# Performance work log

Measured on AMD Instinct MI355X. Metric: run time of the kernel, lower is better.

Reference implementation:

```python
import jax, jax.numpy as jnp
import numpy as np

IN_F, OUT_F, BLOCK, NBLK = 1024, 4096, 256, 16
TOPK = NBLK // 4  # 4, as in forward: n_blocks // 4


def setup_inputs() -> dict:
    key = jax.random.key(0)
    ks = jax.random.split(key, 7)
    s = 1.0 / np.sqrt(IN_F)
    s2 = 1.0 / np.sqrt(OUT_F)
    return {
        "x": jax.random.normal(ks[0], (4, 4096, IN_F), jnp.float32),
        "router_w": jax.random.uniform(ks[1], (NBLK, IN_F), jnp.float32, -s, s),
        "router_b": jax.random.uniform(ks[2], (NBLK,), jnp.float32, -s, s),
        "w1": jax.random.uniform(ks[3], (OUT_F, IN_F), jnp.float32, -s, s),
        "b1": jax.random.uniform(ks[4], (OUT_F,), jnp.float32, -s, s),
        "w2": jax.random.uniform(ks[5], (IN_F, OUT_F), jnp.float32, -s2, s2),
        "b2": jax.random.uniform(ks[6], (IN_F,), jnp.float32, -s2, s2),
    }


def reference(x, router_w, router_b, w1, b1, w2, b2):
    x_shape = x.shape
    xf = x.reshape(-1, IN_F)  # [N, d]
    n = xf.shape[0]
    # router: Linear + softmax, then top-k block selection per token
    prob = jax.nn.softmax(xf @ router_w.T + router_b, axis=-1)  # [N, n_blocks]
    _, idx = jax.lax.top_k(prob, TOPK)  # [N, k]
    mask = jnp.zeros((n, NBLK), bool).at[jnp.arange(n)[:, None], idx].set(True)
    # RoutedLinearRow: per-block fc1, zeros at unselected blocks
    w1b = w1.reshape(NBLK, BLOCK, IN_F)
    b1b = b1.reshape(NBLK, BLOCK)
    h = jnp.einsum('nd,ibd->nib', xf, w1b) + b1b  # [N, n_blocks, block]
    h = jnp.where(mask[:, :, None], h, jnp.zeros((), h.dtype))
    h = jax.nn.relu(h)
    # RoutedLinearCol: only selected blocks contribute
    w2b = w2.reshape(IN_F, NBLK, BLOCK)
    y = jnp.einsum('nib,dib->nd', jnp.where(mask[:, :, None], h, 0.0), w2b) + b2
    return y.reshape(x_shape)
```

## Files before the change

### kernel.cpp

```cpp
#include <hip/hip_runtime.h>
#include <hip/hip_bf16.h>

#define NTOK   16384
#define INF    1024
#define OUTF   4096
#define NBLK   16
#define BLKSZ  256
#define KTOP   4

typedef short bf16x8 __attribute__((ext_vector_type(8)));
typedef float f32x4 __attribute__((ext_vector_type(4)));
typedef unsigned short u16x8 __attribute__((ext_vector_type(8)));

__device__ __forceinline__ unsigned short f2bf(float f) {
  unsigned u = __float_as_uint(f);
  u += 0x7FFFu + ((u >> 16) & 1u);
  return (unsigned short)(u >> 16);
}

__device__ __forceinline__ void load_lds16(const void* g, void* l) {
  __builtin_amdgcn_global_load_lds(
      (const __attribute__((address_space(1))) unsigned int*)g,
      (__attribute__((address_space(3))) unsigned int*)l, 16, 0, 0);
}

__device__ __forceinline__ double shfl_xor_d(double v, int m) {
  long long l = __double_as_longlong(v);
  int lo = (int)(l & 0xFFFFFFFFll), hi = (int)(l >> 32);
  lo = __shfl_xor(lo, m);
  hi = __shfl_xor(hi, m);
  return __longlong_as_double(((long long)hi << 32) | (unsigned long long)(unsigned)lo);
}

__device__ __forceinline__ int pi_perm(int j) {
  return (j & 128) | ((j & 7) << 4) | ((j >> 3) & 15);
}

__global__ void k_zero(unsigned* __restrict__ list32, unsigned* __restrict__ counts) {
  int i = blockIdx.x * 256 + threadIdx.x;
  if (i < 33792) list32[i] = 0;
  else if (i < 33808) counts[i - 33792] = 0;
}

__global__ __launch_bounds__(256) void k_convert(
    const float* __restrict__ w1, const float* __restrict__ w2,
    const float* __restrict__ b1, unsigned short* __restrict__ w1b,
    unsigned short* __restrict__ w2p, float* __restrict__ b1p) {
  const size_t stride = (size_t)gridDim.x * 256;
  for (size_t i = (size_t)blockIdx.x * 256 + threadIdx.x; i < 1573376; i += stride) {
    if (i < 1048576) {
      float4 v = ((const float4*)w1)[i];
      ushort4 o;
      o.x = f2bf(v.x); o.y = f2bf(v.y); o.z = f2bf(v.z); o.w = f2bf(v.w);
      ((ushort4*)w1b)[i] = o;
    } else if (i < 1572864) {
      const size_t g = i - 1048576;
      const int d = (int)(g >> 9);
      const int rest = (int)(g & 511);
      const int jg = rest * 8;
      const int blk = jg >> 8;
      const int j0 = jg & 255;
      const float* src = w2 + (size_t)d * 4096 + blk * 256;
      u16x8 o;
#pragma unroll
      for (int ni = 0; ni < 8; ++ni) o[ni] = f2bf(src[pi_perm(j0 + ni)]);
      *(u16x8*)(w2p + (size_t)d * 4096 + jg) = o;
    } else {
      const int idx = (int)(i - 1572864);
      const int jg = idx * 8;
      const int blk = jg >> 8;
      const int j0 = jg & 255;
      const float* src = b1 + blk * 256;
      float o[8];
#pragma unroll
      for (int ni = 0; ni < 8; ++ni) o[ni] = src[pi_perm(j0 + ni)];
      float4* dst = (float4*)(b1p + jg);
      dst[0] = make_float4(o[0], o[1], o[2], o[3]);
      dst[1] = make_float4(o[4], o[5], o[6], o[7]);
    }
  }
}

__global__ __launch_bounds__(256) void k_router(
    const float* __restrict__ x, const float* __restrict__ rw,
    const float* __restrict__ rb, unsigned* __restrict__ tok_blocks,
    unsigned* __restrict__ counts, unsigned short* __restrict__ xb) {
  __shared__ float4 rwl[4096];
  const int tid = threadIdx.x;
  const float4* rw4 = (const float4*)rw;
  for (int i = tid; i < 4096; i += 256) rwl[i] = rw4[i];
  __syncthreads();

  const int n = blockIdx.x * 32 + (tid >> 3);
  const int q = tid & 7;
  double p[16];
#pragma unroll
  for (int j = 0; j < 16; ++j) p[j] = 0.0;
  const float4* xr = (const float4*)(x + (size_t)n * INF);
  ushort4* xbr = (ushort4*)(xb + (size_t)n * INF);
#pragma unroll 4
  for (int i = 0; i < 32; ++i) {
    const int d4 = q + i * 8;
    const float4 xv = xr[d4];
    ushort4 o;
    o.x = f2bf(xv.x); o.y = f2bf(xv.y); o.z = f2bf(xv.z); o.w = f2bf(xv.w);
    xbr[d4] = o;
#pragma unroll
    for (int j = 0; j < 16; ++j) {
      const float4 wv = rwl[j * 256 + d4];
      p[j] = fma((double)xv.x, (double)wv.x, p[j]);
      p[j] = fma((double)xv.y, (double)wv.y, p[j]);
      p[j] = fma((double)xv.z, (double)wv.z, p[j]);
      p[j] = fma((double)xv.w, (double)wv.w, p[j]);
    }
  }
#pragma unroll
  for (int j = 0; j < 16; ++j) {
    double v = p[j];
    v += shfl_xor_d(v, 1);
    v += shfl_xor_d(v, 2);
    v += shfl_xor_d(v, 4);
    p[j] = v + (double)rb[j];
  }

  __syncthreads();
  unsigned* hist = (unsigned*)rwl;
  if (tid < 16) hist[tid] = 0;
  __syncthreads();

  if (q == 0) {
    unsigned packed = 0;
#pragma unroll
    for (int j = 0; j < 16; ++j) {
      int r = 0;
#pragma unroll
      for (int j2 = 0; j2 < 16; ++j2)
        r += (int)((p[j2] > p[j]) | ((p[j2] == p[j]) & (j2 < j)));
      if (r < KTOP) packed |= (unsigned)j << (8 * r);
    }
    tok_blocks[n] = packed;
    atomicAdd(&hist[packed & 15u], 1u);
    atomicAdd(&hist[(packed >> 8) & 15u], 1u);
    atomicAdd(&hist[(packed >> 16) & 15u], 1u);
    atomicAdd(&hist[(packed >> 24) & 15u], 1u);
  }
  __syncthreads();
  if (tid < 16 && hist[tid]) atomicAdd(&counts[tid], hist[tid]);
}

__global__ void k_scan(const unsigned* __restrict__ counts, unsigned* __restrict__ off,
                       unsigned* __restrict__ cursors) {
  if (threadIdx.x == 0 && blockIdx.x == 0) {
    unsigned o = 0;
    for (int i = 0; i < 16; ++i) {
      off[i] = o; cursors[i] = o;
      o += (counts[i] + 127u) & ~127u;
    }
    off[16] = o;
  }
}

__global__ __launch_bounds__(256) void k_build(
    const unsigned* __restrict__ tok_blocks, unsigned* __restrict__ cursors,
    unsigned short* __restrict__ list, unsigned* __restrict__ inv) {
  const int n = blockIdx.x * 256 + threadIdx.x;
  const unsigned packed = tok_blocks[n];
  const int lane = threadIdx.x & 63;
  for (int b = 0; b < 16; ++b) {
    int r = -1;
#pragma unroll
    for (int q = 0; q < 4; ++q)
      if (((packed >> (8 * q)) & 15u) == (unsigned)b) r = q;
    unsigned long long m = __ballot(r >= 0);
    if (m) {
      int leader = __ffsll((unsigned long long)m) - 1;
      unsigned base = 0;
      if (lane == leader) base = atomicAdd(&cursors[b], (unsigned)__popcll(m));
      base = (unsigned)__shfl((int)base, leader);
      if (r >= 0) {
        unsigned pos = base + (unsigned)__popcll(m & ((1ull << lane) - 1ull));
        list[pos] = (unsigned short)n;
        inv[(size_t)n * 4 + r] = pos;
      }
    }
  }
}

__global__ __launch_bounds__(512, 1) void k_ffn(
    const unsigned short* __restrict__ xb, const unsigned short* __restrict__ w1b,
    const unsigned short* __restrict__ w2p, const float* __restrict__ b1p,
    const unsigned short* __restrict__ list, const unsigned* __restrict__ counts,
    const unsigned* __restrict__ off, unsigned short* __restrict__ part) {
  __shared__ __align__(16) char lds[163840];
  char* const As0 = lds + 65536;
  char* const As1 = lds + 81920;
  char* const Bs0 = lds + 98304;
  char* const Bs1 = lds + 131072;

  const int bid0 = blockIdx.x;
  const int bid = (bid0 & 7) * 256 + (bid0 >> 3);
  const int blk = bid >> 7;
  const int tile = bid & 127;
  const unsigned cnt = counts[blk];
  if ((unsigned)(tile * 128) >= cnt) return;
  const unsigned goff = off[blk] + tile * 128;

  const int tid = threadIdx.x;
  const int lane = tid & 63;
  const int wid = tid >> 6;
  const int wr = wid >> 1;
  const int wc = wid & 1;
  const int asl = tid & 7;
  const int c16 = lane & 15;

  const unsigned tok0 = list[goff + (tid >> 3)];
  const unsigned tok1 = list[goff + 64 + (tid >> 3)];
  const int arow0 = tid >> 3;
  const int arow1 = 64 + arow0;

#define STAGE_A(buf, k0)                                                        \
  {                                                                             \
    load_lds16(xb + (size_t)tok0 * INF + (k0) + (asl ^ (arow0 & 7)) * 8,        \
               (buf) + (wid * 64) * 16);                                        \
    load_lds16(xb + (size_t)tok1 * INF + (k0) + (asl ^ (arow1 & 7)) * 8,        \
               (buf) + (512 + wid * 64) * 16);                                  \
  }

#define STAGE_B1(buf, k0)                                                       \
  _Pragma("unroll")                                                             \
  for (int r = 0; r < 4; ++r) {                                                 \
    const int row = (r * 512 + tid) >> 3;                                       \
    load_lds16(w1b + ((size_t)(blk * 256 + row)) * INF + (k0) +                 \
                   (asl ^ (row & 7)) * 8,                                       \
               (buf) + (r * 512 + wid * 64) * 16);                              \
  }

#define COMPUTE_A(abuf, bbuf)                                                   \
  _Pragma("unroll")                                                             \
  for (int ks = 0; ks < 2; ++ks) {                                              \
    const int kc = ks * 4 + (lane >> 4);                                        \
    bf16x8 a[2], b[8];                                                          \
    _Pragma("unroll")                                                           \
    for (int mi = 0; mi < 2; ++mi) {                                            \
      const int row = wr * 32 + mi * 16 + (lane & 15);                          \
      a[mi] = *(const bf16x8*)((abuf) + row * 128 + ((kc ^ (row & 7)) << 4));   \
    }                                                                           \
    _Pragma("unroll")                                                           \
    for (int ni = 0; ni < 8; ++ni) {                                            \
      const int row = wc * 128 + ni * 16 + (lane & 15);                         \
      b[ni] = *(const bf16x8*)((bbuf) + row * 128 + ((kc ^ (row & 7)) << 4));   \
    }                                                                           \
    _Pragma("unroll")                                                           \
    for (int mi = 0; mi < 2; ++mi)                                              \
      _Pragma("unroll")                                                         \
      for (int ni = 0; ni < 8; ++ni)                                            \
        acc[mi][ni] =                                                           \
            __builtin_amdgcn_mfma_f32_16x16x32_bf16(a[mi], b[ni], acc[mi][ni], 0, 0, 0); \
  }

  f32x4 acc[2][8] = {};
  STAGE_A(As0, 0);
  STAGE_B1(Bs0, 0);
  __syncthreads();
#pragma unroll 1
  for (int kk = 0; kk < 8; ++kk) {
    const int k0 = kk * 128;
    STAGE_A(As1, k0 + 64);
    STAGE_B1(Bs1, k0 + 64);
    COMPUTE_A(As0, Bs0);
    __syncthreads();
    if (kk < 7) {
      STAGE_A(As0, k0 + 128);
      STAGE_B1(Bs0, k0 + 128);
    }
    COMPUTE_A(As1, Bs1);
    __syncthreads();
  }

#define STAGE_B2(buf, it)                                                       \
  {                                                                             \
    const int ns2 = (it) >> 2, k02 = ((it) & 3) * 64;                           \
    _Pragma("unroll")                                                           \
    for (int r = 0; r < 4; ++r) {                                               \
      const int row = (r * 512 + tid) >> 3;                                     \
      load_lds16(w2p + (size_t)(ns2 * 256 + row) * OUTF + blk * 256 + k02 +     \
                     (asl ^ (row & 7)) * 8,                                     \
                 (buf) + (r * 512 + wid * 64) * 16);                            \
    }                                                                           \
  }

#define COMPUTE_B(bbuf, k02)                                                    \
  _Pragma("unroll")                                                             \
  for (int ks = 0; ks < 2; ++ks) {                                              \
    const int kc = ks * 4 + (lane >> 4);                                        \
    bf16x8 a[2], b[8];                                                          \
    _Pragma("unroll")                                                           \
    for (int mi = 0; mi < 2; ++mi) {                                            \
      const int row = wr * 32 + mi * 16 + (lane & 15);                          \
      a[mi] = *(const bf16x8*)(lds + row * 512 + (k02) * 2 +                    \
                               ((kc ^ (row & 7)) << 4));                        \
    }                                                                           \
    _Pragma("unroll")                                                           \
    for (int ni = 0; ni < 8; ++ni) {                                            \
      const int row = wc * 128 + ni * 16 + (lane & 15);                         \
      b[ni] = *(const bf16x8*)((bbuf) + row * 128 + ((kc ^ (row & 7)) << 4));   \
    }                                                                           \
    _Pragma("unroll")                                                           \
    for (int mi = 0; mi < 2; ++mi)                                              \
      _Pragma("unroll")                                                         \
      for (int ni = 0; ni < 8; ++ni)                                            \
        acc2[mi][ni] =                                                          \
            __builtin_amdgcn_mfma_f32_16x16x32_bf16(a[mi], b[ni], acc2[mi][ni], 0, 0, 0); \
  }

  STAGE_B2(Bs0, 0);

  {
    const float4* bp = (const float4*)(b1p + blk * 256 + wc * 128 + c16 * 8);
    const float4 bv0 = bp[0], bv1 = bp[1];
    const float bvv[8] = {bv0.x, bv0.y, bv0.z, bv0.w, bv1.x, bv1.y, bv1.z, bv1.w};
    const int chunk = wc * 16 + c16;
    const int cslot = (chunk & ~7);
    const int clow  = (chunk & 7);
#pragma unroll
    for (int mi = 0; mi < 2; ++mi) {
#pragma unroll
      for (int i = 0; i < 4; ++i) {
        const int row = wr * 32 + mi * 16 + (lane >> 4) * 4 + i;
        u16x8 wv;
#pragma unroll
        for (int ni = 0; ni < 8; ++ni) {
          float v = acc[mi][ni][i] + bvv[ni];
          v = v > 0.f ? v : 0.f;
          wv[ni] = f2bf(v);
        }
        *(u16x8*)(lds + row * 512 + ((cslot | (clow ^ (row & 7))) << 4)) = wv;
      }
    }
  }
  __syncthreads();

#pragma unroll 1
  for (int ns = 0; ns < 4; ++ns) {
    f32x4 acc2[2][8] = {};
    const int it0 = ns * 4;
    STAGE_B2(Bs1, it0 + 1);
    COMPUTE_B(Bs0, 0);
    __syncthreads();
    STAGE_B2(Bs0, it0 + 2);
    COMPUTE_B(Bs1, 64);
    __syncthreads();
    STAGE_B2(Bs1, it0 + 3);
    COMPUTE_B(Bs0, 128);
    __syncthreads();
    if (ns < 3) STAGE_B2(Bs0, it0 + 4);
    COMPUTE_B(Bs1, 192);
    __syncthreads();
#pragma unroll
    for (int mi = 0; mi < 2; ++mi) {
#pragma unroll
      for (int i = 0; i < 4; ++i) {
        const int row = wr * 32 + mi * 16 + (lane >> 4) * 4 + i;
        u16x8 wv;
#pragma unroll
        for (int ni = 0; ni < 8; ++ni) wv[ni] = f2bf(acc2[mi][ni][i]);
        *(u16x8*)(part + (size_t)(goff + row) * 1024 + ns * 256 + wc * 128 + c16 * 8) = wv;
      }
    }
  }
#undef STAGE_A
#undef STAGE_B1
#undef STAGE_B2
#undef COMPUTE_A
#undef COMPUTE_B
}

__global__ __launch_bounds__(256) void k_reduce(const unsigned short* __restrict__ part,
                                                const unsigned* __restrict__ inv,
                                                const float* __restrict__ b2,
                                                float* __restrict__ out) {
  __shared__ float lds[8 * 1028];
  const int tid = threadIdx.x;
  const int tok0 = blockIdx.x * 8;
  const int tok_l = tid >> 5;
  const int l32 = tid & 31;

  const uint4 iv = *(const uint4*)(inv + (size_t)(tok0 + tok_l) * 4);
  const unsigned prow[4] = {iv.x, iv.y, iv.z, iv.w};

#pragma unroll
  for (int g = 0; g < 4; ++g) {
    const int idx = g * 32 + l32;
    const int p0 = idx * 8;
    float s[8] = {0.f, 0.f, 0.f, 0.f, 0.f, 0.f, 0.f, 0.f};
#pragma unroll
    for (int sl = 0; sl < 4; ++sl) {
      u16x8 v = *(const u16x8*)(part + (size_t)prow[sl] * 1024 + p0);
#pragma unroll
      for (int j = 0; j < 8; ++j)
        s[j] += __uint_as_float((unsigned)(unsigned short)v[j] << 16);
    }
    const int ns = idx >> 5, wcb = (idx >> 4) & 1, cc = idx & 15;
#pragma unroll
    for (int ni = 0; ni < 8; ++ni)
      lds[tok_l * 1028 + ns * 256 + wcb * 128 + ni * 16 + cc] = s[ni];
  }
  __syncthreads();
  const float4 b2v = ((const float4*)b2)[tid];
#pragma unroll
  for (int r = 0; r < 8; ++r) {
    f32x4 lv = *(f32x4*)&lds[r * 1028 + tid * 4];
    float4 o = make_float4(lv[0] + b2v.x, lv[1] + b2v.y, lv[2] + b2v.z, lv[3] + b2v.w);
    *(float4*)(out + (size_t)(tok0 + r) * 1024 + tid * 4) = o;
  }
}

extern "C" void kernel_launch(void* const* d_in, const int* in_sizes, int n_in,
                              void* d_out, int out_size, void* d_ws, size_t ws_size,
                              hipStream_t stream) {
  const float* x  = (const float*)d_in[0];
  const float* rw = (const float*)d_in[1];
  const float* rb = (const float*)d_in[2];
  const float* w1 = (const float*)d_in[3];
  const float* b1 = (const float*)d_in[4];
  const float* w2 = (const float*)d_in[5];
  const float* b2 = (const float*)d_in[6];
  float* out = (float*)d_out;

  char* ws = (char*)d_ws;
  unsigned short* part = (unsigned short*)(ws);
  unsigned short* xb   = (unsigned short*)(ws + 138412032);
  unsigned short* w1b  = (unsigned short*)(ws + 171966464);
  unsigned short* w2p  = (unsigned short*)(ws + 180355072);
  unsigned* tokb       = (unsigned*)(ws + 188743680);
  unsigned short* list = (unsigned short*)(ws + 188809216);
  unsigned* inv        = (unsigned*)(ws + 188944384);
  float* b1p           = (float*)(ws + 189206528);
  unsigned* counts     = (unsigned*)(ws + 189222912);
  unsigned* off        = (unsigned*)(ws + 189222976);
  unsigned* cursors    = (unsigned*)(ws + 189223104);

  k_zero<<<dim3(133), dim3(256), 0, stream>>>((unsigned*)list, counts);
  k_convert<<<dim3(1024), dim3(256), 0, stream>>>(w1, w2, b1, w1b, w2p, b1p);
  k_router<<<dim3(512), dim3(256), 0, stream>>>(x, rw, rb, tokb, counts, xb);
  k_scan<<<dim3(1), dim3(64), 0, stream>>>(counts, off, cursors);
  k_build<<<dim3(64), dim3(256), 0, stream>>>(tokb, cursors, list, inv);
  k_ffn<<<dim3(2048), dim3(512), 0, stream>>>(xb, w1b, w2p, b1p, list, counts, off, part);
  k_reduce<<<dim3(2048), dim3(256), 0, stream>>>(part, inv, b2, out);
}
```

Before: 266.7 us.

## Triple-buffer FFN tiles with K=32 steps and one barrier per step

Rewrites both GEMM phases of the routed FFN kernel to use a three-deep LDS ring of K=32 slices in place of double-buffered K=64 slices. Explicit vmcnt waits and a single s_barrier per step replace the paired __syncthreads, so global-to-LDS loads for step t+2 are in flight while step t computes. The swizzle changes to a 64-byte row layout and total LDS drops. This shortens each MFMA burst per barrier and relies on hand-tuned vmcnt counts being correct, which is fragile.

```diff
diff --git a/kernel.cpp b/kernel.cpp
--- a/kernel.cpp
+++ b/kernel.cpp
@@ -191,11 +191,7 @@
     const unsigned short* __restrict__ w2p, const float* __restrict__ b1p,
     const unsigned short* __restrict__ list, const unsigned* __restrict__ counts,
     const unsigned* __restrict__ off, unsigned short* __restrict__ part) {
-  __shared__ __align__(16) char lds[163840];
-  char* const As0 = lds + 65536;
-  char* const As1 = lds + 81920;
-  char* const Bs0 = lds + 98304;
-  char* const Bs1 = lds + 131072;
+  __shared__ __align__(16) char lds[139264];
 
   const int bid0 = blockIdx.x;
   const int bid = (bid0 & 7) * 256 + (bid0 >> 3);
@@ -210,110 +206,106 @@
   const int wid = tid >> 6;
   const int wr = wid >> 1;
   const int wc = wid & 1;
-  const int asl = tid & 7;
   const int c16 = lane & 15;
-
-  const unsigned tok0 = list[goff + (tid >> 3)];
-  const unsigned tok1 = list[goff + 64 + (tid >> 3)];
-  const int arow0 = tid >> 3;
-  const int arow1 = 64 + arow0;
-
-#define STAGE_A(buf, k0)                                                        \
+  const int kc4 = lane >> 4;
+
+  const unsigned tokA = list[goff + (tid >> 2)];
+  const int aChunk = (tid & 3) ^ ((tid >> 3) & 3);
+
+#define VMF asm volatile("" ::: "memory")
+#define BAR __builtin_amdgcn_s_barrier()
+
+#define STAGE_A(buf, k0_)                                                       \
   {                                                                             \
-    load_lds16(xb + (size_t)tok0 * INF + (k0) + (asl ^ (arow0 & 7)) * 8,        \
-               (buf) + (wid * 64) * 16);                                        \
-    load_lds16(xb + (size_t)tok1 * INF + (k0) + (asl ^ (arow1 & 7)) * 8,        \
-               (buf) + (512 + wid * 64) * 16);                                  \
-  }
-
-#define STAGE_B1(buf, k0)                                                       \
-  _Pragma("unroll")                                                             \
-  for (int r = 0; r < 4; ++r) {                                                 \
-    const int row = (r * 512 + tid) >> 3;                                       \
-    load_lds16(w1b + ((size_t)(blk * 256 + row)) * INF + (k0) +                 \
-                   (asl ^ (row & 7)) * 8,                                       \
-               (buf) + (r * 512 + wid * 64) * 16);                              \
-  }
-
-#define COMPUTE_A(abuf, bbuf)                                                   \
-  _Pragma("unroll")                                                             \
-  for (int ks = 0; ks < 2; ++ks) {                                              \
-    const int kc = ks * 4 + (lane >> 4);                                        \
+    load_lds16(xb + (size_t)tokA * 1024 + (k0_) + aChunk * 8, (buf) + tid * 16);\
+    _Pragma("unroll")                                                           \
+    for (int l = 0; l < 2; ++l) {                                               \
+      const int idx = l * 512 + tid;                                            \
+      load_lds16(w1b + (size_t)(blk * 256 + (idx >> 2)) * 1024 + (k0_) +        \
+                     (((idx & 3) ^ ((idx >> 3) & 3)) * 8),                      \
+                 (buf) + 8192 + idx * 16);                                      \
+    }                                                                           \
+  }
+
+#define COMPUTE_A(buf)                                                          \
+  {                                                                             \
     bf16x8 a[2], b[8];                                                          \
     _Pragma("unroll")                                                           \
     for (int mi = 0; mi < 2; ++mi) {                                            \
       const int row = wr * 32 + mi * 16 + (lane & 15);                          \
-      a[mi] = *(const bf16x8*)((abuf) + row * 128 + ((kc ^ (row & 7)) << 4));   \
+      a[mi] = *(const bf16x8*)((buf) + row * 64 +                               \
+                               ((kc4 ^ ((row >> 1) & 3)) << 4));                \
     }                                                                           \
     _Pragma("unroll")                                                           \
     for (int ni = 0; ni < 8; ++ni) {                                            \
       const int row = wc * 128 + ni * 16 + (lane & 15);                         \
-      b[ni] = *(const bf16x8*)((bbuf) + row * 128 + ((kc ^ (row & 7)) << 4));   \
+      b[ni] = *(const bf16x8*)((buf) + 8192 + row * 64 +                        \
+                               ((kc4 ^ ((row >> 1) & 3)) << 4));                \
     }                                                                           \
     _Pragma("unroll")                                                           \
     for (int mi = 0; mi < 2; ++mi)                                              \
       _Pragma("unroll")                                                         \
       for (int ni = 0; ni < 8; ++ni)                                            \
-        acc[mi][ni] =                                                           \
-            __builtin_amdgcn_mfma_f32_16x16x32_bf16(a[mi], b[ni], acc[mi][ni], 0, 0, 0); \
-  }
-
+        acc[mi][ni] = __builtin_amdgcn_mfma_f32_16x16x32_bf16(a[mi], b[ni],     \
+                                                   acc[mi][ni], 0, 0, 0);       \
+  }
+
+  char* bA0 = lds + 65536;
+  char* bA1 = lds + 90112;
+  char* bA2 = lds + 114688;
   f32x4 acc[2][8] = {};
-  STAGE_A(As0, 0);
-  STAGE_B1(Bs0, 0);
-  __syncthreads();
+  STAGE_A(bA0, 0);
+  STAGE_A(bA1, 32);
 #pragma unroll 1
-  for (int kk = 0; kk < 8; ++kk) {
-    const int k0 = kk * 128;
-    STAGE_A(As1, k0 + 64);
-    STAGE_B1(Bs1, k0 + 64);
-    COMPUTE_A(As0, Bs0);
-    __syncthreads();
-    if (kk < 7) {
-      STAGE_A(As0, k0 + 128);
-      STAGE_B1(Bs0, k0 + 128);
-    }
-    COMPUTE_A(As1, Bs1);
-    __syncthreads();
-  }
-
-#define STAGE_B2(buf, it)                                                       \
+  for (int t = 0; t < 32; ++t) {
+    if (t < 31) { asm volatile("s_waitcnt vmcnt(3)" ::: "memory"); }
+    else        { asm volatile("s_waitcnt vmcnt(0)" ::: "memory"); }
+    BAR; VMF;
+    if (t < 30) STAGE_A(bA2, (t + 2) * 32);
+    COMPUTE_A(bA0);
+    char* tmp = bA0; bA0 = bA1; bA1 = bA2; bA2 = tmp;
+  }
+
+#define STAGE_B(buf, it_)                                                       \
   {                                                                             \
-    const int ns2 = (it) >> 2, k02 = ((it) & 3) * 64;                           \
-    _Pragma("unroll")                                                           \
-    for (int r = 0; r < 4; ++r) {                                               \
-      const int row = (r * 512 + tid) >> 3;                                     \
-      load_lds16(w2p + (size_t)(ns2 * 256 + row) * OUTF + blk * 256 + k02 +     \
-                     (asl ^ (row & 7)) * 8,                                     \
-                 (buf) + (r * 512 + wid * 64) * 16);                            \
-    }                                                                           \
-  }
-
-#define COMPUTE_B(bbuf, k02)                                                    \
-  _Pragma("unroll")                                                             \
-  for (int ks = 0; ks < 2; ++ks) {                                              \
-    const int kc = ks * 4 + (lane >> 4);                                        \
+    const int ns2 = (it_) >> 3, k02 = ((it_) & 7) * 32;                         \
+    _Pragma("unroll")                                                           \
+    for (int l = 0; l < 2; ++l) {                                               \
+      const int idx = l * 512 + tid;                                            \
+      load_lds16(w2p + (size_t)(ns2 * 256 + (idx >> 2)) * 4096 + blk * 256 +    \
+                     k02 + (((idx & 3) ^ ((idx >> 3) & 3)) * 8),                \
+                 (buf) + idx * 16);                                             \
+    }                                                                           \
+  }
+
+#define COMPUTE_B(buf, t_)                                                      \
+  {                                                                             \
+    const int cgl = ((t_) & 7) * 4 + kc4;                                       \
     bf16x8 a[2], b[8];                                                          \
     _Pragma("unroll")                                                           \
     for (int mi = 0; mi < 2; ++mi) {                                            \
       const int row = wr * 32 + mi * 16 + (lane & 15);                          \
-      a[mi] = *(const bf16x8*)(lds + row * 512 + (k02) * 2 +                    \
-                               ((kc ^ (row & 7)) << 4));                        \
+      const int slot = (cgl & ~7) | ((cgl & 7) ^ (row & 7));                    \
+      a[mi] = *(const bf16x8*)(lds + row * 512 + slot * 16);                    \
     }                                                                           \
     _Pragma("unroll")                                                           \
     for (int ni = 0; ni < 8; ++ni) {                                            \
       const int row = wc * 128 + ni * 16 + (lane & 15);                         \
-      b[ni] = *(const bf16x8*)((bbuf) + row * 128 + ((kc ^ (row & 7)) << 4));   \
+      b[ni] = *(const bf16x8*)((buf) + row * 64 +                               \
+                               ((kc4 ^ ((row >> 1) & 3)) << 4));                \
     }                                                                           \
     _Pragma("unroll")                                                           \
     for (int mi = 0; mi < 2; ++mi)                                              \
       _Pragma("unroll")                                                         \
       for (int ni = 0; ni < 8; ++ni)                                            \
-        acc2[mi][ni] =                                                          \
-            __builtin_amdgcn_mfma_f32_16x16x32_bf16(a[mi], b[ni], acc2[mi][ni], 0, 0, 0); \
-  }
-
-  STAGE_B2(Bs0, 0);
+        acc2[mi][ni] = __builtin_amdgcn_mfma_f32_16x16x32_bf16(a[mi], b[ni],    \
+                                                    acc2[mi][ni], 0, 0, 0);     \
+  }
+
+  char* bB0 = lds + 65536;
+  char* bB1 = lds + 81920;
+  char* bB2 = lds + 98304;
+  STAGE_B(bB0, 0);
 
   {
     const float4* bp = (const float4*)(b1p + blk * 256 + wc * 128 + c16 * 8);
@@ -338,41 +330,44 @@
       }
     }
   }
-  __syncthreads();
-
+  asm volatile("s_waitcnt lgkmcnt(0)" ::: "memory");
+  BAR; VMF;
+  STAGE_B(bB1, 1);
+
+  f32x4 acc2[2][8] = {};
 #pragma unroll 1
-  for (int ns = 0; ns < 4; ++ns) {
-    f32x4 acc2[2][8] = {};
-    const int it0 = ns * 4;
-    STAGE_B2(Bs1, it0 + 1);
-    COMPUTE_B(Bs0, 0);
-    __syncthreads();
-    STAGE_B2(Bs0, it0 + 2);
-    COMPUTE_B(Bs1, 64);
-    __syncthreads();
-    STAGE_B2(Bs1, it0 + 3);
-    COMPUTE_B(Bs0, 128);
-    __syncthreads();
-    if (ns < 3) STAGE_B2(Bs0, it0 + 4);
-    COMPUTE_B(Bs1, 192);
-    __syncthreads();
-#pragma unroll
-    for (int mi = 0; mi < 2; ++mi) {
-#pragma unroll
-      for (int i = 0; i < 4; ++i) {
-        const int row = wr * 32 + mi * 16 + (lane >> 4) * 4 + i;
-        u16x8 wv;
-#pragma unroll
-        for (int ni = 0; ni < 8; ++ni) wv[ni] = f2bf(acc2[mi][ni][i]);
-        *(u16x8*)(part + (size_t)(goff + row) * 1024 + ns * 256 + wc * 128 + c16 * 8) = wv;
+  for (int t = 0; t < 32; ++t) {
+    if (t == 31)                   { asm volatile("s_waitcnt vmcnt(0)" ::: "memory"); }
+    else if ((t & 7) == 0 && t > 0){ asm volatile("s_waitcnt vmcnt(10)" ::: "memory"); }
+    else                           { asm volatile("s_waitcnt vmcnt(2)" ::: "memory"); }
+    BAR; VMF;
+    if (t < 30) STAGE_B(bB2, t + 2);
+    COMPUTE_B(bB0, t);
+    if ((t & 7) == 7) {
+      const int nsq = t >> 3;
+#pragma unroll
+      for (int mi = 0; mi < 2; ++mi) {
+#pragma unroll
+        for (int i = 0; i < 4; ++i) {
+          const int row = wr * 32 + mi * 16 + (lane >> 4) * 4 + i;
+          u16x8 wv;
+#pragma unroll
+          for (int ni = 0; ni < 8; ++ni) wv[ni] = f2bf(acc2[mi][ni][i]);
+          *(u16x8*)(part + (size_t)(goff + row) * 1024 + nsq * 256 +
+                    wc * 128 + c16 * 8) = wv;
+#pragma unroll
+          for (int ni = 0; ni < 8; ++ni) acc2[mi][ni][i] = 0.f;
+        }
       }
     }
+    char* tmp = bB0; bB0 = bB1; bB1 = bB2; bB2 = tmp;
   }
 #undef STAGE_A
-#undef STAGE_B1
-#undef STAGE_B2
+#undef STAGE_B
 #undef COMPUTE_A
 #undef COMPUTE_B
+#undef VMF
+#undef BAR
 }
 
 __global__ __launch_bounds__(256) void k_reduce(const unsigned short* __restrict__ part,
```

Result: slower. 275.2 us (+3.2%).

## Scatter FFN partials to token-major layout and drop inverse index and zero kernel

Applied to the files above, without the earlier changes.

The FFN epilogue now writes each partial output row directly to a token-major slot (token*4 + rank), with the rank packed into the upper bits of the 16-bit list entry. The reduce kernel can then read four contiguous rows per token with no inverse index array. The separate zeroing kernel is removed and the counter reset moves into k_convert. Padded rows are skipped through a bounds check, which replaces zero-filling the list. The epilogue stores become scattered instead of contiguous, and correctness depends on token ids fitting in 14 bits.

```diff
diff --git a/kernel.cpp b/kernel.cpp
--- a/kernel.cpp
+++ b/kernel.cpp
@@ -36,16 +36,12 @@
   return (j & 128) | ((j & 7) << 4) | ((j >> 3) & 15);
 }
 
-__global__ void k_zero(unsigned* __restrict__ list32, unsigned* __restrict__ counts) {
-  int i = blockIdx.x * 256 + threadIdx.x;
-  if (i < 33792) list32[i] = 0;
-  else if (i < 33808) counts[i - 33792] = 0;
-}
-
 __global__ __launch_bounds__(256) void k_convert(
     const float* __restrict__ w1, const float* __restrict__ w2,
     const float* __restrict__ b1, unsigned short* __restrict__ w1b,
-    unsigned short* __restrict__ w2p, float* __restrict__ b1p) {
+    unsigned short* __restrict__ w2p, float* __restrict__ b1p,
+    unsigned* __restrict__ counts) {
+  if (blockIdx.x == 0 && threadIdx.x < 16) counts[threadIdx.x] = 0;
   const size_t stride = (size_t)gridDim.x * 256;
   for (size_t i = (size_t)blockIdx.x * 256 + threadIdx.x; i < 1573376; i += stride) {
     if (i < 1048576) {
@@ -162,7 +158,7 @@
 
 __global__ __launch_bounds__(256) void k_build(
     const unsigned* __restrict__ tok_blocks, unsigned* __restrict__ cursors,
-    unsigned short* __restrict__ list, unsigned* __restrict__ inv) {
+    unsigned short* __restrict__ list) {
   const int n = blockIdx.x * 256 + threadIdx.x;
   const unsigned packed = tok_blocks[n];
   const int lane = threadIdx.x & 63;
@@ -179,8 +175,7 @@
       base = (unsigned)__shfl((int)base, leader);
       if (r >= 0) {
         unsigned pos = base + (unsigned)__popcll(m & ((1ull << lane) - 1ull));
-        list[pos] = (unsigned short)n;
-        inv[(size_t)n * 4 + r] = pos;
+        list[pos] = (unsigned short)(n | (r << 14));
       }
     }
   }
@@ -204,6 +199,7 @@
   const unsigned cnt = counts[blk];
   if ((unsigned)(tile * 128) >= cnt) return;
   const unsigned goff = off[blk] + tile * 128;
+  const int rem = (int)cnt - tile * 128;
 
   const int tid = threadIdx.x;
   const int lane = tid & 63;
@@ -213,10 +209,17 @@
   const int asl = tid & 7;
   const int c16 = lane & 15;
 
-  const unsigned tok0 = list[goff + (tid >> 3)];
-  const unsigned tok1 = list[goff + 64 + (tid >> 3)];
+  const unsigned tok0 = list[goff + (tid >> 3)] & 0x3FFFu;
+  const unsigned tok1 = list[goff + 64 + (tid >> 3)] & 0x3FFFu;
   const int arow0 = tid >> 3;
   const int arow1 = 64 + arow0;
+
+  unsigned ep[2][4];
+#pragma unroll
+  for (int mi = 0; mi < 2; ++mi)
+#pragma unroll
+    for (int i = 0; i < 4; ++i)
+      ep[mi][i] = list[goff + wr * 32 + mi * 16 + (lane >> 4) * 4 + i];
 
 #define STAGE_A(buf, k0)                                                        \
   {                                                                             \
@@ -361,10 +364,14 @@
 #pragma unroll
       for (int i = 0; i < 4; ++i) {
         const int row = wr * 32 + mi * 16 + (lane >> 4) * 4 + i;
-        u16x8 wv;
-#pragma unroll
-        for (int ni = 0; ni < 8; ++ni) wv[ni] = f2bf(acc2[mi][ni][i]);
-        *(u16x8*)(part + (size_t)(goff + row) * 1024 + ns * 256 + wc * 128 + c16 * 8) = wv;
+        if (row < rem) {
+          const unsigned e = ep[mi][i];
+          u16x8 wv;
+#pragma unroll
+          for (int ni = 0; ni < 8; ++ni) wv[ni] = f2bf(acc2[mi][ni][i]);
+          *(u16x8*)(part + ((size_t)(e & 0x3FFFu) * 4 + (e >> 14)) * 1024 +
+                    ns * 256 + wc * 128 + c16 * 8) = wv;
+        }
       }
     }
   }
@@ -376,7 +383,6 @@
 }
 
 __global__ __launch_bounds__(256) void k_reduce(const unsigned short* __restrict__ part,
-                                                const unsigned* __restrict__ inv,
                                                 const float* __restrict__ b2,
                                                 float* __restrict__ out) {
   __shared__ float lds[8 * 1028];
@@ -384,9 +390,7 @@
   const int tok0 = blockIdx.x * 8;
   const int tok_l = tid >> 5;
   const int l32 = tid & 31;
-
-  const uint4 iv = *(const uint4*)(inv + (size_t)(tok0 + tok_l) * 4);
-  const unsigned prow[4] = {iv.x, iv.y, iv.z, iv.w};
+  const unsigned short* pbase = part + (size_t)(tok0 + tok_l) * 4096;
 
 #pragma unroll
   for (int g = 0; g < 4; ++g) {
@@ -395,7 +399,7 @@
     float s[8] = {0.f, 0.f, 0.f, 0.f, 0.f, 0.f, 0.f, 0.f};
 #pragma unroll
     for (int sl = 0; sl < 4; ++sl) {
-      u16x8 v = *(const u16x8*)(part + (size_t)prow[sl] * 1024 + p0);
+      u16x8 v = *(const u16x8*)(pbase + sl * 1024 + p0);
 #pragma unroll
       for (int j = 0; j < 8; ++j)
         s[j] += __uint_as_float((unsigned)(unsigned short)v[j] << 16);
@@ -429,22 +433,20 @@
 
   char* ws = (char*)d_ws;
   unsigned short* part = (unsigned short*)(ws);
-  unsigned short* xb   = (unsigned short*)(ws + 138412032);
-  unsigned short* w1b  = (unsigned short*)(ws + 171966464);
-  unsigned short* w2p  = (unsigned short*)(ws + 180355072);
-  unsigned* tokb       = (unsigned*)(ws + 188743680);
-  unsigned short* list = (unsigned short*)(ws + 188809216);
-  unsigned* inv        = (unsigned*)(ws + 188944384);
-  float* b1p           = (float*)(ws + 189206528);
-  unsigned* counts     = (unsigned*)(ws + 189222912);
-  unsigned* off        = (unsigned*)(ws + 189222976);
-  unsigned* cursors    = (unsigned*)(ws + 189223104);
-
-  k_zero<<<dim3(133), dim3(256), 0, stream>>>((unsigned*)list, counts);
-  k_convert<<<dim3(1024), dim3(256), 0, stream>>>(w1, w2, b1, w1b, w2p, b1p);
+  unsigned short* xb   = (unsigned short*)(ws + 134217728);
+  unsigned short* w1b  = (unsigned short*)(ws + 167772160);
+  unsigned short* w2p  = (unsigned short*)(ws + 176160768);
+  unsigned* tokb       = (unsigned*)(ws + 184549376);
+  unsigned short* list = (unsigned short*)(ws + 184614912);
+  float* b1p           = (float*)(ws + 184750080);
+  unsigned* counts     = (unsigned*)(ws + 184766464);
+  unsigned* off        = (unsigned*)(ws + 184766528);
+  unsigned* cursors    = (unsigned*)(ws + 184766656);
+
+  k_convert<<<dim3(1024), dim3(256), 0, stream>>>(w1, w2, b1, w1b, w2p, b1p, counts);
   k_router<<<dim3(512), dim3(256), 0, stream>>>(x, rw, rb, tokb, counts, xb);
   k_scan<<<dim3(1), dim3(64), 0, stream>>>(counts, off, cursors);
-  k_build<<<dim3(64), dim3(256), 0, stream>>>(tokb, cursors, list, inv);
+  k_build<<<dim3(64), dim3(256), 0, stream>>>(tokb, cursors, list);
   k_ffn<<<dim3(2048), dim3(512), 0, stream>>>(xb, w1b, w2p, b1p, list, counts, off, part);
-  k_reduce<<<dim3(2048), dim3(256), 0, stream>>>(part, inv, b2, out);
-}
+  k_reduce<<<dim3(2048), dim3(256), 0, stream>>>(part, b2, out);
+}
```

Result: faster. 260.2 us (-2.4%).
